# Kernel tuning notes

Measured on AMD Instinct MI355X. Metric: run time of the kernel, lower is better.

## Reference

```python
import jax, jax.numpy as jnp
import numpy as np
import math

N, C, L, D = 8, 16, 1024, 7   # x: [N, in_heads=C, L, in_features=D]
H = 16                        # out_heads
SZ = C * D                    # 112 (in_sz == out_sz since in_heads == out_heads)

def setup_inputs() -> dict:
    key = jax.random.key(0)
    ks = jax.random.split(key, 7)
    s = 1.0 / math.sqrt(SZ)
    return {
        "x":  jax.random.normal(ks[0], (N, C, L, D), dtype=jnp.float32),
        "Wq": jax.random.normal(ks[1], (SZ, SZ), dtype=jnp.float32) * s,
        "bq": jax.random.normal(ks[2], (SZ,), dtype=jnp.float32) * s,
        "Wk": jax.random.normal(ks[3], (SZ, SZ), dtype=jnp.float32) * s,
        "bk": jax.random.normal(ks[4], (SZ,), dtype=jnp.float32) * s,
        "Wv": jax.random.normal(ks[5], (SZ, SZ), dtype=jnp.float32) * s,
        "bv": jax.random.normal(ks[6], (SZ,), dtype=jnp.float32) * s,
    }

def _split_heads(t):
    # [N, L, H*d] -> [N, H, L, d]
    n, l, _ = t.shape
    return t.reshape(n, l, H, -1).transpose(0, 2, 1, 3)

def reference(x, Wq, bq, Wk, bk, Wv, bv):
    n, c, l, d = x.shape
    # [N, C, L, D] -> [N, L, C*D]
    xf = x.transpose(0, 2, 1, 3).reshape(n, l, c * d)
    q = _split_heads(xf @ Wq.T + bq)   # [N, H, L, d]
    k = _split_heads(xf @ Wk.T + bk)
    v = _split_heads(xf @ Wv.T + bv)
    scores = jnp.einsum('bhqd,bhkd->bhqk', q, k)
    # NOTE: original scales by sqrt(scores.shape[-1]) == sqrt(L), not sqrt(head_dim)
    scores = scores / jnp.sqrt(jnp.asarray(l, scores.dtype))
    weights = jax.nn.softmax(scores.astype(jnp.float32), axis=-1).astype(scores.dtype)
    # dropout p=0.5 is identity in eval mode
    return jnp.einsum('bhqk,bhkd->bhqd', weights, v)
```

## Files before the change

kernel.cpp:

```cpp
#include <hip/hip_runtime.h>
#include <math.h>

#define NB 8
#define CH 16
#define LL 1024
#define DD 7
#define HH 16

typedef float  v2f  __attribute__((ext_vector_type(2)));
typedef float  v4f  __attribute__((ext_vector_type(4)));
typedef float  v16f __attribute__((ext_vector_type(16)));
typedef short  v8s  __attribute__((ext_vector_type(8)));

#if __has_builtin(__builtin_amdgcn_exp2f)
#define EXP2F(x) __builtin_amdgcn_exp2f(x)
#else
#define EXP2F(x) exp2f(x)
#endif

__device__ inline unsigned bf16_rne(float f) {
    unsigned u = __builtin_bit_cast(unsigned, f);
    return (u + 0x7fffu + ((u >> 16) & 1u)) >> 16;
}
__device__ inline unsigned pack_trunc(float a, float b) {
    unsigned ua = __builtin_bit_cast(unsigned, a);
    unsigned ub = __builtin_bit_cast(unsigned, b);
    return (ua >> 16) | (ub & 0xffff0000u);
}

__global__ __launch_bounds__(256, 2) void qkv_proj(
    const float* __restrict__ x,
    const float* __restrict__ Wq, const float* __restrict__ bq,
    const float* __restrict__ Wk, const float* __restrict__ bk,
    const float* __restrict__ Wv, const float* __restrict__ bv,
    unsigned short* __restrict__ qkvb)
{
    __shared__ __align__(16) float Ws[112 * 112];
    __shared__ __align__(16) float xt[64 * 116];

    int bx  = blockIdx.x;
    int mat = bx / (NB * 16);
    int rem = bx % (NB * 16);
    int n   = rem / 16;
    int l0  = (rem % 16) * 64;

    const float* W = (mat == 0) ? Wq : (mat == 1) ? Wk : Wv;
    const float* b = (mat == 0) ? bq : (mat == 1) ? bk : bv;

    int tid = threadIdx.x;

    {
        const uint4* src = (const uint4*)W;
        uint4* dst = (uint4*)Ws;
        for (int i = tid; i < 3136; i += 256) dst[i] = src[i];
    }
    for (int idx = tid; idx < 64 * 112; idx += 256) {
        int c  = idx / 448;
        int r  = idx - c * 448;
        int l  = r / 7;
        int dd = r - l * 7;
        xt[l * 116 + c * 7 + dd] = x[((n * CH + c) * LL + l0 + l) * DD + dd];
    }
    __syncthreads();

    int jh = tid >> 4;
    int lg = tid & 15;

    v2f acc2[2][7];
    #pragma unroll
    for (int j = 0; j < 7; ++j) {
        float bj = b[jh * 7 + j];
        acc2[0][j] = (v2f){bj, bj};
        acc2[1][j] = (v2f){bj, bj};
    }

    const v4f* Wv4 = (const v4f*)Ws;
    const v4f* Xv4 = (const v4f*)xt;

    for (int i4 = 0; i4 < 28; ++i4) {
        v4f wv[7];
        #pragma unroll
        for (int j = 0; j < 7; ++j) wv[j] = Wv4[(jh * 7 + j) * 28 + i4];
        v4f x0 = Xv4[(0  + lg) * 29 + i4];
        v4f x1 = Xv4[(16 + lg) * 29 + i4];
        v4f x2 = Xv4[(32 + lg) * 29 + i4];
        v4f x3 = Xv4[(48 + lg) * 29 + i4];
        #pragma unroll
        for (int f = 0; f < 4; ++f) {
            v2f xa = (v2f){x0[f], x1[f]};
            v2f xb = (v2f){x2[f], x3[f]};
            #pragma unroll
            for (int j = 0; j < 7; ++j) {
                v2f wj = (v2f){wv[j][f], wv[j][f]};
                acc2[0][j] += xa * wj;
                acc2[1][j] += xb * wj;
            }
        }
    }

    const float scale = (mat == 0) ? 0.0450842200277801f  : 1.0f;
    #pragma unroll
    for (int rp = 0; rp < 2; ++rp) {
        #pragma unroll
        for (int e = 0; e < 2; ++e) {
            int r = rp * 2 + e;
            float a0 = acc2[rp][0][e] * scale, a1 = acc2[rp][1][e] * scale;
            float a2 = acc2[rp][2][e] * scale, a3 = acc2[rp][3][e] * scale;
            float a4 = acc2[rp][4][e] * scale, a5 = acc2[rp][5][e] * scale;
            float a6 = acc2[rp][6][e] * scale;
            unsigned d0 = bf16_rne(a0) | (bf16_rne(a1) << 16);
            unsigned d1 = bf16_rne(a2) | (bf16_rne(a3) << 16);
            unsigned d2 = bf16_rne(a4) | (bf16_rne(a5) << 16);
            unsigned d3 = bf16_rne(a6);
            int row = l0 + r * 16 + lg;
            uint4* dst = (uint4*)qkvb + ((size_t)(mat * NB + n) * HH + jh) * LL + row;
            *dst = make_uint4(d0, d1, d2, d3);
        }
    }
}

__global__ __launch_bounds__(256, 2) void attn(
    const unsigned short* __restrict__ qkvb, float* __restrict__ out)
{
    __shared__ __align__(16) unsigned short Kl[LL * 8];
    __shared__ __align__(16) unsigned short Vt[8 * 1040];
    __shared__ __align__(16) unsigned short Pb[4 * 64 * 40];

    int bx = blockIdx.x;
    int qt = bx & 3, h = (bx >> 2) & 15, n = bx >> 6;
    int tid  = threadIdx.x;
    int wave = tid >> 6, lane = tid & 63;
    int l31 = lane & 31, g5 = lane >> 5, l15 = lane & 15, l4 = lane >> 4;

    const unsigned short* Qg = qkvb + (size_t)((0 * NB + n) * HH + h) * (LL * 8);
    const unsigned short* Kg = qkvb + (size_t)((1 * NB + n) * HH + h) * (LL * 8);
    const unsigned short* Vg = qkvb + (size_t)((2 * NB + n) * HH + h) * (LL * 8);

    {
        const uint4* Ks = (const uint4*)Kg;
        const uint4* Vs = (const uint4*)Vg;
        uint4* Kd = (uint4*)Kl;
        uint4* Vd = (uint4*)Pb;
        #pragma unroll
        for (int it = 0; it < 4; ++it) {
            int i = tid + it * 256;
            Kd[i] = Ks[i];
            Vd[i] = Vs[i];
        }
    }
    __syncthreads();

    {
        const uint4* Vd = (const uint4*)Pb;
        uint4 r0 = Vd[4 * tid], r1 = Vd[4 * tid + 1];
        uint4 r2 = Vd[4 * tid + 2], r3 = Vd[4 * tid + 3];
        const unsigned* p0 = (const unsigned*)&r0;
        const unsigned* p1 = (const unsigned*)&r1;
        const unsigned* p2 = (const unsigned*)&r2;
        const unsigned* p3 = (const unsigned*)&r3;
        int col = ((tid >> 3) << 5) + ((tid & 1) << 4) + (((tid >> 1) & 3) << 2);
        #pragma unroll
        for (int d = 0; d < 7; ++d) {
            unsigned a0 = p0[d >> 1], a1 = p1[d >> 1], a2 = p2[d >> 1], a3 = p3[d >> 1];
            unsigned w0, w1;
            if (d & 1) { w0 = (a0 >> 16) | (a1 & 0xffff0000u); w1 = (a2 >> 16) | (a3 & 0xffff0000u); }
            else       { w0 = (a0 & 0xffffu) | (a1 << 16);     w1 = (a2 & 0xffffu) | (a3 << 16); }
            *(uint2*)&Vt[d * 1040 + col] = make_uint2(w0, w1);
        }
        *(uint2*)&Vt[7 * 1040 + col] = make_uint2(0x3f803f80u, 0x3f803f80u);
    }
    __syncthreads();

    int qbase = qt * 256 + wave * 64;
    v8s zero8 = {0, 0, 0, 0, 0, 0, 0, 0};
    v8s qf0 = (lane < 32) ? *(const v8s*)(Qg + (size_t)(qbase + l31) * 8)      : zero8;
    v8s qf1 = (lane < 32) ? *(const v8s*)(Qg + (size_t)(qbase + 32 + l31) * 8) : zero8;

    v4f acc[4];
    #pragma unroll
    for (int st = 0; st < 4; ++st) acc[st] = (v4f){0.f, 0.f, 0.f, 0.f};

    unsigned short* Pw = Pb + wave * (64 * 40);

    #pragma unroll 2
    for (int c = 0; c < 32; ++c) {
        v8s kf = (lane < 32) ? *(const v8s*)(Kl + (c * 32 + l31) * 8) : zero8;
        v16f s0 = __builtin_amdgcn_mfma_f32_32x32x16_bf16(kf, qf0, (v16f){}, 0, 0, 0);
        v16f s1 = __builtin_amdgcn_mfma_f32_32x32x16_bf16(kf, qf1, (v16f){}, 0, 0, 0);
        {
            unsigned short* dst = Pw + l31 * 40 + (g5 << 4);
            uint4 wa, wb;
            wa.x = pack_trunc(EXP2F(s0[0]),  EXP2F(s0[1]));
            wa.y = pack_trunc(EXP2F(s0[2]),  EXP2F(s0[3]));
            wa.z = pack_trunc(EXP2F(s0[4]),  EXP2F(s0[5]));
            wa.w = pack_trunc(EXP2F(s0[6]),  EXP2F(s0[7]));
            wb.x = pack_trunc(EXP2F(s0[8]),  EXP2F(s0[9]));
            wb.y = pack_trunc(EXP2F(s0[10]), EXP2F(s0[11]));
            wb.z = pack_trunc(EXP2F(s0[12]), EXP2F(s0[13]));
            wb.w = pack_trunc(EXP2F(s0[14]), EXP2F(s0[15]));
            *(uint4*)dst       = wa;
            *(uint4*)(dst + 8) = wb;
        }
        {
            unsigned short* dst = Pw + (32 + l31) * 40 + (g5 << 4);
            uint4 wa, wb;
            wa.x = pack_trunc(EXP2F(s1[0]),  EXP2F(s1[1]));
            wa.y = pack_trunc(EXP2F(s1[2]),  EXP2F(s1[3]));
            wa.z = pack_trunc(EXP2F(s1[4]),  EXP2F(s1[5]));
            wa.w = pack_trunc(EXP2F(s1[6]),  EXP2F(s1[7]));
            wb.x = pack_trunc(EXP2F(s1[8]),  EXP2F(s1[9]));
            wb.y = pack_trunc(EXP2F(s1[10]), EXP2F(s1[11]));
            wb.z = pack_trunc(EXP2F(s1[12]), EXP2F(s1[13]));
            wb.w = pack_trunc(EXP2F(s1[14]), EXP2F(s1[15]));
            *(uint4*)dst       = wa;
            *(uint4*)(dst + 8) = wb;
        }
        v8s vf = (l15 < 8) ? *(const v8s*)(Vt + l15 * 1040 + c * 32 + l4 * 8) : zero8;
        #pragma unroll
        for (int st = 0; st < 4; ++st) {
            v8s pf = *(const v8s*)(Pw + (st * 16 + l15) * 40 + l4 * 8);
            acc[st] = __builtin_amdgcn_mfma_f32_16x16x32_bf16(pf, vf, acc[st], 0, 0, 0);
        }
    }

    size_t obase = (size_t)(n * HH + h) * LL * 7;
    #pragma unroll
    for (int st = 0; st < 4; ++st) {
        #pragma unroll
        for (int r = 0; r < 4; ++r) {
            float val = acc[st][r];
            float rs  = __shfl(val, 7, 16);
            if (l15 < 7)
                out[obase + (size_t)(qbase + st * 16 + l4 * 4 + r) * 7 + l15] = val / rs;
        }
    }
}

extern "C" void kernel_launch(void* const* d_in, const int* in_sizes, int n_in,
                              void* d_out, int out_size, void* d_ws, size_t ws_size,
                              hipStream_t stream) {
    const float* x  = (const float*)d_in[0];
    const float* Wq = (const float*)d_in[1];
    const float* bq = (const float*)d_in[2];
    const float* Wk = (const float*)d_in[3];
    const float* bk = (const float*)d_in[4];
    const float* Wv = (const float*)d_in[5];
    const float* bv = (const float*)d_in[6];
    unsigned short* qkvb = (unsigned short*)d_ws;
    float* o = (float*)d_out;

    qkv_proj<<<dim3(3 * NB * 16), dim3(256), 0, stream>>>(x, Wq, bq, Wk, bk, Wv, bv, qkvb);
    attn<<<dim3(NB * HH * 4), dim3(256), 0, stream>>>(qkvb, o);
}
```

Measured before the change: 110.4 us.

## Software-pipeline attention loop with double-buffered P tile and K prefetch

Restructures the attention inner loop so the PV MFMAs for chunk c-1 run while chunk c's scores are exponentiated and stored, using a double-buffered per-wave P buffer. K fragments are prefetched one iteration ahead. V is transposed straight from global memory instead of staging through shared memory, which drops one sync. The P row stride shrinks from 40 to 36 shorts so two buffers fit, which may change LDS bank-conflict behaviour and raises register pressure.

```diff
diff --git a/kernel.cpp b/kernel.cpp
--- a/kernel.cpp
+++ b/kernel.cpp
@@ -124,7 +124,7 @@
 {
     __shared__ __align__(16) unsigned short Kl[LL * 8];
     __shared__ __align__(16) unsigned short Vt[8 * 1040];
-    __shared__ __align__(16) unsigned short Pb[4 * 64 * 40];
+    __shared__ __align__(16) unsigned short Pb[2 * 4 * 64 * 36];
 
     int bx = blockIdx.x;
     int qt = bx & 3, h = (bx >> 2) & 15, n = bx >> 6;
@@ -138,22 +138,14 @@
 
     {
         const uint4* Ks = (const uint4*)Kg;
+        uint4* Kd = (uint4*)Kl;
+        #pragma unroll
+        for (int it = 0; it < 4; ++it) Kd[tid + it * 256] = Ks[tid + it * 256];
+    }
+    {
         const uint4* Vs = (const uint4*)Vg;
-        uint4* Kd = (uint4*)Kl;
-        uint4* Vd = (uint4*)Pb;
-        #pragma unroll
-        for (int it = 0; it < 4; ++it) {
-            int i = tid + it * 256;
-            Kd[i] = Ks[i];
-            Vd[i] = Vs[i];
-        }
-    }
-    __syncthreads();
-
-    {
-        const uint4* Vd = (const uint4*)Pb;
-        uint4 r0 = Vd[4 * tid], r1 = Vd[4 * tid + 1];
-        uint4 r2 = Vd[4 * tid + 2], r3 = Vd[4 * tid + 3];
+        uint4 r0 = Vs[4 * tid], r1 = Vs[4 * tid + 1];
+        uint4 r2 = Vs[4 * tid + 2], r3 = Vs[4 * tid + 3];
         const unsigned* p0 = (const unsigned*)&r0;
         const unsigned* p1 = (const unsigned*)&r1;
         const unsigned* p2 = (const unsigned*)&r2;
@@ -180,15 +172,20 @@
     #pragma unroll
     for (int st = 0; st < 4; ++st) acc[st] = (v4f){0.f, 0.f, 0.f, 0.f};
 
-    unsigned short* Pw = Pb + wave * (64 * 40);
+    v8s kf  = (lane < 32) ? *(const v8s*)(Kl + l31 * 8) : zero8;
+    v8s vfp = zero8;
 
     #pragma unroll 2
     for (int c = 0; c < 32; ++c) {
-        v8s kf = (lane < 32) ? *(const v8s*)(Kl + (c * 32 + l31) * 8) : zero8;
         v16f s0 = __builtin_amdgcn_mfma_f32_32x32x16_bf16(kf, qf0, (v16f){}, 0, 0, 0);
         v16f s1 = __builtin_amdgcn_mfma_f32_32x32x16_bf16(kf, qf1, (v16f){}, 0, 0, 0);
+
+        v8s kfn = (c < 31 && lane < 32) ? *(const v8s*)(Kl + ((c + 1) * 32 + l31) * 8) : zero8;
+        v8s vfc = (l15 < 8) ? *(const v8s*)(Vt + l15 * 1040 + c * 32 + l4 * 8) : zero8;
+
+        unsigned short* Pw = Pb + ((c & 1) * 4 + wave) * (64 * 36);
         {
-            unsigned short* dst = Pw + l31 * 40 + (g5 << 4);
+            unsigned short* dst = Pw + l31 * 36 + (g5 << 4);
             uint4 wa, wb;
             wa.x = pack_trunc(EXP2F(s0[0]),  EXP2F(s0[1]));
             wa.y = pack_trunc(EXP2F(s0[2]),  EXP2F(s0[3]));
@@ -202,7 +199,7 @@
             *(uint4*)(dst + 8) = wb;
         }
         {
-            unsigned short* dst = Pw + (32 + l31) * 40 + (g5 << 4);
+            unsigned short* dst = Pw + (32 + l31) * 36 + (g5 << 4);
             uint4 wa, wb;
             wa.x = pack_trunc(EXP2F(s1[0]),  EXP2F(s1[1]));
             wa.y = pack_trunc(EXP2F(s1[2]),  EXP2F(s1[3]));
@@ -215,11 +212,24 @@
             *(uint4*)dst       = wa;
             *(uint4*)(dst + 8) = wb;
         }
-        v8s vf = (l15 < 8) ? *(const v8s*)(Vt + l15 * 1040 + c * 32 + l4 * 8) : zero8;
+
+        if (c > 0) {
+            const unsigned short* Pr = Pb + (((c - 1) & 1) * 4 + wave) * (64 * 36);
+            #pragma unroll
+            for (int st = 0; st < 4; ++st) {
+                v8s pf = *(const v8s*)(Pr + (st * 16 + l15) * 36 + l4 * 8);
+                acc[st] = __builtin_amdgcn_mfma_f32_16x16x32_bf16(pf, vfp, acc[st], 0, 0, 0);
+            }
+        }
+        kf  = kfn;
+        vfp = vfc;
+    }
+    {
+        const unsigned short* Pr = Pb + ((31 & 1) * 4 + wave) * (64 * 36);
         #pragma unroll
         for (int st = 0; st < 4; ++st) {
-            v8s pf = *(const v8s*)(Pw + (st * 16 + l15) * 40 + l4 * 8);
-            acc[st] = __builtin_amdgcn_mfma_f32_16x16x32_bf16(pf, vf, acc[st], 0, 0, 0);
+            v8s pf = *(const v8s*)(Pr + (st * 16 + l15) * 36 + l4 * 8);
+            acc[st] = __builtin_amdgcn_mfma_f32_16x16x32_bf16(pf, vfp, acc[st], 0, 0, 0);
         }
     }
 
```

Result: slower. 148.7 us (+34.8%).

## Keep softmax probabilities in registers and feed PV MFMA directly, skipping LDS

Applied to the files above, without the earlier changes.

The attention kernel now packs the exp2 scores straight from the QK^T MFMA accumulator into bf16 operand registers for a 32x32x16 PV MFMA, removing the per-wave LDS round trip for P. This relies on V being laid out in a transposed, permuted order so the register layout matches. Each wave now handles 32 queries instead of 64, and the grid doubles to 8 query tiles per head. The V staging buffer is gone, K fragments are prefetched one step ahead, and launch bounds are raised to 4 blocks per CU to increase occupancy. The trade-off is more blocks, each reloading K and V into LDS, and half the QK MFMA reuse per K fragment.

```diff
diff --git a/kernel.cpp b/kernel.cpp
--- a/kernel.cpp
+++ b/kernel.cpp
@@ -7,10 +7,11 @@
 #define DD 7
 #define HH 16
 
-typedef float  v2f  __attribute__((ext_vector_type(2)));
-typedef float  v4f  __attribute__((ext_vector_type(4)));
-typedef float  v16f __attribute__((ext_vector_type(16)));
-typedef short  v8s  __attribute__((ext_vector_type(8)));
+typedef float    v2f  __attribute__((ext_vector_type(2)));
+typedef float    v4f  __attribute__((ext_vector_type(4)));
+typedef float    v16f __attribute__((ext_vector_type(16)));
+typedef short    v8s  __attribute__((ext_vector_type(8)));
+typedef unsigned v4u  __attribute__((ext_vector_type(4)));
 
 #if __has_builtin(__builtin_amdgcn_exp2f)
 #define EXP2F(x) __builtin_amdgcn_exp2f(x)
@@ -119,18 +120,17 @@
     }
 }
 
-__global__ __launch_bounds__(256, 2) void attn(
+__global__ __launch_bounds__(256, 4) void attn(
     const unsigned short* __restrict__ qkvb, float* __restrict__ out)
 {
     __shared__ __align__(16) unsigned short Kl[LL * 8];
-    __shared__ __align__(16) unsigned short Vt[8 * 1040];
-    __shared__ __align__(16) unsigned short Pb[4 * 64 * 40];
+    __shared__ __align__(16) unsigned short Vt[8 * 1048];
 
     int bx = blockIdx.x;
-    int qt = bx & 3, h = (bx >> 2) & 15, n = bx >> 6;
+    int qt = bx & 7, h = (bx >> 3) & 15, n = bx >> 7;
     int tid  = threadIdx.x;
     int wave = tid >> 6, lane = tid & 63;
-    int l31 = lane & 31, g5 = lane >> 5, l15 = lane & 15, l4 = lane >> 4;
+    int l31 = lane & 31, g5 = lane >> 5;
 
     const unsigned short* Qg = qkvb + (size_t)((0 * NB + n) * HH + h) * (LL * 8);
     const unsigned short* Kg = qkvb + (size_t)((1 * NB + n) * HH + h) * (LL * 8);
@@ -138,101 +138,66 @@
 
     {
         const uint4* Ks = (const uint4*)Kg;
+        uint4* Kd = (uint4*)Kl;
+        #pragma unroll
+        for (int it = 0; it < 4; ++it) Kd[tid + it * 256] = Ks[tid + it * 256];
+    }
+    {
         const uint4* Vs = (const uint4*)Vg;
-        uint4* Kd = (uint4*)Kl;
-        uint4* Vd = (uint4*)Pb;
-        #pragma unroll
-        for (int it = 0; it < 4; ++it) {
-            int i = tid + it * 256;
-            Kd[i] = Ks[i];
-            Vd[i] = Vs[i];
-        }
-    }
-    __syncthreads();
-
-    {
-        const uint4* Vd = (const uint4*)Pb;
-        uint4 r0 = Vd[4 * tid], r1 = Vd[4 * tid + 1];
-        uint4 r2 = Vd[4 * tid + 2], r3 = Vd[4 * tid + 3];
+        uint4 r0 = Vs[4 * tid], r1 = Vs[4 * tid + 1];
+        uint4 r2 = Vs[4 * tid + 2], r3 = Vs[4 * tid + 3];
         const unsigned* p0 = (const unsigned*)&r0;
         const unsigned* p1 = (const unsigned*)&r1;
         const unsigned* p2 = (const unsigned*)&r2;
         const unsigned* p3 = (const unsigned*)&r3;
-        int col = ((tid >> 3) << 5) + ((tid & 1) << 4) + (((tid >> 1) & 3) << 2);
+        int col = ((tid >> 3) << 5) + ((tid & 1) << 3) + (((tid >> 1) & 1) << 2)
+                + (((tid >> 2) & 1) << 4);
         #pragma unroll
         for (int d = 0; d < 7; ++d) {
             unsigned a0 = p0[d >> 1], a1 = p1[d >> 1], a2 = p2[d >> 1], a3 = p3[d >> 1];
             unsigned w0, w1;
             if (d & 1) { w0 = (a0 >> 16) | (a1 & 0xffff0000u); w1 = (a2 >> 16) | (a3 & 0xffff0000u); }
             else       { w0 = (a0 & 0xffffu) | (a1 << 16);     w1 = (a2 & 0xffffu) | (a3 << 16); }
-            *(uint2*)&Vt[d * 1040 + col] = make_uint2(w0, w1);
+            *(uint2*)&Vt[d * 1048 + col] = make_uint2(w0, w1);
         }
-        *(uint2*)&Vt[7 * 1040 + col] = make_uint2(0x3f803f80u, 0x3f803f80u);
+        *(uint2*)&Vt[7 * 1048 + col] = make_uint2(0x3f803f80u, 0x3f803f80u);
     }
     __syncthreads();
 
-    int qbase = qt * 256 + wave * 64;
+    int q = qt * 128 + wave * 32 + l31;
     v8s zero8 = {0, 0, 0, 0, 0, 0, 0, 0};
-    v8s qf0 = (lane < 32) ? *(const v8s*)(Qg + (size_t)(qbase + l31) * 8)      : zero8;
-    v8s qf1 = (lane < 32) ? *(const v8s*)(Qg + (size_t)(qbase + 32 + l31) * 8) : zero8;
-
-    v4f acc[4];
+    v8s qf = (lane < 32) ? *(const v8s*)(Qg + (size_t)q * 8) : zero8;
+
+    const unsigned short* Vrow = Vt + (l31 & 7) * 1048 + g5 * 8;
+    v16f acc = {};
+
+    v8s kf = (lane < 32) ? *(const v8s*)(Kl + l31 * 8) : zero8;
+
+    #pragma unroll 4
+    for (int c = 0; c < 32; ++c) {
+        v16f s = __builtin_amdgcn_mfma_f32_32x32x16_bf16(kf, qf, (v16f){}, 0, 0, 0);
+        if (c < 31)
+            kf = (lane < 32) ? *(const v8s*)(Kl + ((c + 1) * 32 + l31) * 8) : zero8;
+        v8s va1 = *(const v8s*)(Vrow + c * 32);
+        v8s va2 = *(const v8s*)(Vrow + c * 32 + 16);
+
+        unsigned pk[8];
+        #pragma unroll
+        for (int p = 0; p < 8; ++p)
+            pk[p] = pack_trunc(EXP2F(s[2 * p]), EXP2F(s[2 * p + 1]));
+        v8s pA = __builtin_bit_cast(v8s, (v4u){pk[0], pk[1], pk[2], pk[3]});
+        v8s pB = __builtin_bit_cast(v8s, (v4u){pk[4], pk[5], pk[6], pk[7]});
+
+        acc = __builtin_amdgcn_mfma_f32_32x32x16_bf16(va1, pA, acc, 0, 0, 0);
+        acc = __builtin_amdgcn_mfma_f32_32x32x16_bf16(va2, pB, acc, 0, 0, 0);
+    }
+
+    float rs = __shfl(acc[3], 32 + l31, 64);
+    float* base = out + (size_t)(n * HH + h) * LL * 7 + (size_t)q * 7;
     #pragma unroll
-    for (int st = 0; st < 4; ++st) acc[st] = (v4f){0.f, 0.f, 0.f, 0.f};
-
-    unsigned short* Pw = Pb + wave * (64 * 40);
-
-    #pragma unroll 2
-    for (int c = 0; c < 32; ++c) {
-        v8s kf = (lane < 32) ? *(const v8s*)(Kl + (c * 32 + l31) * 8) : zero8;
-        v16f s0 = __builtin_amdgcn_mfma_f32_32x32x16_bf16(kf, qf0, (v16f){}, 0, 0, 0);
-        v16f s1 = __builtin_amdgcn_mfma_f32_32x32x16_bf16(kf, qf1, (v16f){}, 0, 0, 0);
-        {
-            unsigned short* dst = Pw + l31 * 40 + (g5 << 4);
-            uint4 wa, wb;
-            wa.x = pack_trunc(EXP2F(s0[0]),  EXP2F(s0[1]));
-            wa.y = pack_trunc(EXP2F(s0[2]),  EXP2F(s0[3]));
-            wa.z = pack_trunc(EXP2F(s0[4]),  EXP2F(s0[5]));
-            wa.w = pack_trunc(EXP2F(s0[6]),  EXP2F(s0[7]));
-            wb.x = pack_trunc(EXP2F(s0[8]),  EXP2F(s0[9]));
-            wb.y = pack_trunc(EXP2F(s0[10]), EXP2F(s0[11]));
-            wb.z = pack_trunc(EXP2F(s0[12]), EXP2F(s0[13]));
-            wb.w = pack_trunc(EXP2F(s0[14]), EXP2F(s0[15]));
-            *(uint4*)dst       = wa;
-            *(uint4*)(dst + 8) = wb;
-        }
-        {
-            unsigned short* dst = Pw + (32 + l31) * 40 + (g5 << 4);
-            uint4 wa, wb;
-            wa.x = pack_trunc(EXP2F(s1[0]),  EXP2F(s1[1]));
-            wa.y = pack_trunc(EXP2F(s1[2]),  EXP2F(s1[3]));
-            wa.z = pack_trunc(EXP2F(s1[4]),  EXP2F(s1[5]));
-            wa.w = pack_trunc(EXP2F(s1[6]),  EXP2F(s1[7]));
-            wb.x = pack_trunc(EXP2F(s1[8]),  EXP2F(s1[9]));
-            wb.y = pack_trunc(EXP2F(s1[10]), EXP2F(s1[11]));
-            wb.z = pack_trunc(EXP2F(s1[12]), EXP2F(s1[13]));
-            wb.w = pack_trunc(EXP2F(s1[14]), EXP2F(s1[15]));
-            *(uint4*)dst       = wa;
-            *(uint4*)(dst + 8) = wb;
-        }
-        v8s vf = (l15 < 8) ? *(const v8s*)(Vt + l15 * 1040 + c * 32 + l4 * 8) : zero8;
-        #pragma unroll
-        for (int st = 0; st < 4; ++st) {
-            v8s pf = *(const v8s*)(Pw + (st * 16 + l15) * 40 + l4 * 8);
-            acc[st] = __builtin_amdgcn_mfma_f32_16x16x32_bf16(pf, vf, acc[st], 0, 0, 0);
-        }
-    }
-
-    size_t obase = (size_t)(n * HH + h) * LL * 7;
-    #pragma unroll
-    for (int st = 0; st < 4; ++st) {
-        #pragma unroll
-        for (int r = 0; r < 4; ++r) {
-            float val = acc[st][r];
-            float rs  = __shfl(val, 7, 16);
-            if (l15 < 7)
-                out[obase + (size_t)(qbase + st * 16 + l4 * 4 + r) * 7 + l15] = val / rs;
-        }
+    for (int r = 0; r < 4; ++r) {
+        int dim = 4 * g5 + r;
+        if (dim < 7) base[dim] = acc[r] / rs;
     }
 }
 
@@ -250,5 +215,5 @@
     float* o = (float*)d_out;
 
     qkv_proj<<<dim3(3 * NB * 16), dim3(256), 0, stream>>>(x, Wq, bq, Wk, bk, Wv, bv, qkvb);
-    attn<<<dim3(NB * HH * 4), dim3(256), 0, stream>>>(qkvb, o);
-}
+    attn<<<dim3(NB * HH * 8), dim3(256), 0, stream>>>(qkvb, o);
+}
```

Result: faster. 106.6 us (-3.4%).
